# Kernel tuning notes

Hardware: AMD Instinct MI355X
Metric: run time of the kernel (lower is better)

The kernel has to match this reference:

```python
import jax, jax.numpy as jnp
import numpy as np

S0, S1 = 256, 256          # spins (up, down)
N = S0 + S1                # total electrons
SINGLE = 256               # single_dim == single_out (residual requires match)
PAIR = 128                 # pair_dim == pair_out
GAIN_TANH = 1.5927812698663017  # ActivationWithGain: 1/std(tanh(N(0,1)))
SQRT2 = 1.4142135623730951


def setup_inputs() -> dict:
    key = jax.random.key(0)
    ks = jax.random.split(key, 7)
    h_one = jax.random.normal(ks[0], (N, SINGLE), jnp.float32)
    h_two = jax.random.normal(ks[1], (N, N, PAIR), jnp.float32)
    din = SINGLE + 2 * PAIR  # one_in feature dim = 512
    # variance_scaling(2, fan_in) kernels; bias ~ Normal(0, sqrt(2))
    W1 = jax.random.normal(ks[2], (din, SINGLE), jnp.float32) * (2.0 / din) ** 0.5
    b1 = jax.random.normal(ks[3], (SINGLE,), jnp.float32) * SQRT2
    Wg = jax.random.normal(ks[4], (2 * SINGLE, SINGLE), jnp.float32) * (2.0 / (2 * SINGLE)) ** 0.5
    W2 = jax.random.normal(ks[5], (PAIR, PAIR), jnp.float32) * (2.0 / PAIR) ** 0.5
    b2 = jax.random.normal(ks[6], (PAIR,), jnp.float32) * SQRT2
    return dict(h_one=h_one, h_two=h_two, W1=W1, b1=b1, Wg=Wg, W2=W2, b2=b2)


def _act(x):
    # ActivationWithGain(tanh): rescale so output variance ~ input variance
    return jnp.tanh(x) * jnp.asarray(GAIN_TANH, x.dtype)


def reference(h_one, h_two, W1, b1, Wg, W2, b2):
    # construct_single_features: per-spin mean of h_two over sender axis
    g2_up = jnp.mean(h_two[:S0], axis=0)            # (N, PAIR)
    g2_dn = jnp.mean(h_two[S0:], axis=0)            # (N, PAIR)
    one_in = jnp.concatenate([h_one, g2_up, g2_dn], axis=1)   # (N, SINGLE+2*PAIR)
    # construct_global_features: per-spin mean of h_one, concat on features
    g1_up = jnp.mean(h_one[:S0], axis=0, keepdims=True)       # (1, SINGLE)
    g1_dn = jnp.mean(h_one[S0:], axis=0, keepdims=True)       # (1, SINGLE)
    global_in = jnp.concatenate([g1_up, g1_dn], axis=-1)      # (1, 2*SINGLE)

    h_one_new = one_in @ W1 + b1 + global_in @ Wg             # (N, SINGLE)
    h_one_new = _act(h_one_new / SQRT2)
    h_one_out = (h_one + h_one_new) / SQRT2                   # residual (shapes match)

    h_two_new = _act(h_two @ W2 + b2)                         # (N, N, PAIR)
    h_two_out = (h_two + h_two_new) / SQRT2                   # residual
    return h_one_out, h_two_out
```

## Files before the change

### kernel.cpp

```cpp
#include <hip/hip_runtime.h>
#include <stdint.h>

#define NN 512
#define PAIR 128
#define SINGLE 256

#define GAINv 1.5927812698663017f
#define RS2 0.70710678118654752f

typedef unsigned int uint;
typedef unsigned short ushort;
typedef short bf16x8 __attribute__((ext_vector_type(8)));
typedef float f32x4 __attribute__((ext_vector_type(4)));

__device__ __forceinline__ ushort f2b(float f){
  union{float f;uint i;}v; v.f=f;
  uint x=v.i;
  return (ushort)((x + 0x7FFFu + ((x>>16)&1u))>>16);
}
__device__ __forceinline__ float b2f_lo(uint u){ union{uint i;float f;}v; v.i=u<<16; return v.f; }
__device__ __forceinline__ float b2f_hi(uint u){ union{uint i;float f;}v; v.i=u&0xFFFF0000u; return v.f; }
__device__ __forceinline__ float tanh_fast(float x){
  float xc = fminf(fmaxf(x,-8.f),8.f);
  float e = __expf(2.f*xc);
  return (e-1.f)*__builtin_amdgcn_rcpf(e+1.f);
}

__global__ __launch_bounds__(256) void k1_prep(const float* __restrict__ h_one,
                                               const float* __restrict__ w2,
                                               float* __restrict__ g1part,
                                               ushort* __restrict__ wt,
                                               float* __restrict__ g2acc)
{
  const int b = blockIdx.x, t = threadIdx.x;
  if(b < 8){
    const int rb = b*64;
    float s = 0.f;
    for(int i=0;i<64;i++) s += h_one[(size_t)(rb+i)*SINGLE + t];
    g1part[b*SINGLE + t] = s;
  } else if(b < 16){
    const int bb = b-8;
    for(int e=t; e<16*128; e+=256){
      int kl = e>>7, n = e&127;
      int k = bb*16 + kl;
      wt[n*128 + k] = f2b(w2[(size_t)k*128 + n]);
    }
  } else {
    f32x4 z = (f32x4){0.f,0.f,0.f,0.f};
    f32x4* dst = (f32x4*)g2acc + (size_t)(b-16)*4096;
    for(int q=t; q<4096; q+=256) dst[q] = z;
  }
}

__global__ __launch_bounds__(256) void k2_gterm(const float* __restrict__ g1part,
                                                const float* __restrict__ wg,
                                                float* __restrict__ gtermpart)
{
  __shared__ float g1m[512];
  const int t = threadIdx.x;
  g1m[t]     = (g1part[t]      + g1part[256+t]  + g1part[512+t]  + g1part[768+t])  * (1.f/256.f);
  g1m[t+256] = (g1part[1024+t] + g1part[1280+t] + g1part[1536+t] + g1part[1792+t]) * (1.f/256.f);
  __syncthreads();
  const int fb = blockIdx.x*64;
  float s = 0.f;
  for(int f=fb; f<fb+64; f++)
    s += g1m[f]*wg[(size_t)f*SINGLE + t];
  gtermpart[blockIdx.x*SINGLE + t] = s;
}

__global__ __launch_bounds__(256, 4) void k3_htwo(
    const float* __restrict__ h_two,
    const float* __restrict__ b2,
    const ushort* __restrict__ wt,
    float* __restrict__ g2acc,
    float* __restrict__ out_h2)
{
  __shared__ __align__(16) ushort At[64*128];
  const int tid = threadIdx.x;
  const int w = tid>>6, lane = tid&63;
  const int lq = lane>>4, lr = lane&15;
  const int bi = blockIdx.x & 31, bj = blockIdx.x >> 5;
  const int i0 = bi*16, j0 = bj*4;
  const int spin = bi>>4;

  #pragma unroll
  for(int rep=0;rep<8;rep++){
    const int e = rep*1024 + tid*4;
    const int di = e>>9, c = e&511;
    const float4 v = *(const float4*)(h_two + ((size_t)(i0+di)*NN + j0)*PAIR + c);
    ushort4 pk; pk.x=f2b(v.x); pk.y=f2b(v.y); pk.z=f2b(v.z); pk.w=f2b(v.w);
    const int r = e>>7;
    *(ushort4*)(&At[e ^ ((r&7)<<3)]) = pk;
  }

  bf16x8 af[2][4];
  #pragma unroll
  for(int nt=0;nt<2;nt++){
    const int n = w*32 + nt*16 + lr;
    #pragma unroll
    for(int kk=0;kk<4;kk++)
      af[nt][kk] = *(const bf16x8*)(wt + n*128 + kk*32 + lq*8);
  }
  f32x4 bias[2];
  #pragma unroll
  for(int nt=0;nt<2;nt++){
    const float4 bv = *(const float4*)(b2 + w*32 + nt*16 + lq*4);
    bias[nt] = (f32x4){bv.x, bv.y, bv.z, bv.w};
  }
  __syncthreads();

  {
    const int dj = w, pp = lane;
    const uint* a32 = (const uint*)At;
    float s0=0.f, s1=0.f;
    #pragma unroll
    for(int di=0;di<16;di++){
      const int r = di*4+dj;
      uint u = a32[(r*64 + pp) ^ ((r&7)<<2)];
      s0 += b2f_lo(u); s1 += b2f_hi(u);
    }
    float* dst = g2acc + ((size_t)spin*NN + (j0+dj))*PAIR + pp*2;
    atomicAdd(dst, s0); atomicAdd(dst+1, s1);
  }

  f32x4 acc[4][2];
  #pragma unroll
  for(int mt=0;mt<4;mt++){
    acc[mt][0] = bias[0];
    acc[mt][1] = bias[1];
  }
  #pragma unroll
  for(int kk=0;kk<4;kk++){
    bf16x8 bfr[4];
    #pragma unroll
    for(int mt=0;mt<4;mt++){
      const int m = mt*16 + lr;
      const int e = m*128 + kk*32 + lq*8;
      bfr[mt] = *(const bf16x8*)(&At[e ^ ((lr&7)<<3)]);
    }
    #pragma unroll
    for(int mt=0;mt<4;mt++){
      acc[mt][0] = __builtin_amdgcn_mfma_f32_16x16x32_bf16(af[0][kk], bfr[mt], acc[mt][0], 0,0,0);
      acc[mt][1] = __builtin_amdgcn_mfma_f32_16x16x32_bf16(af[1][kk], bfr[mt], acc[mt][1], 0,0,0);
    }
  }

  #pragma unroll
  for(int mt=0;mt<4;mt++){
    const int m = mt*16 + lr;
    const size_t base = ((size_t)(i0 + (m>>2))*NN + (j0 + (m&3)))*PAIR;
    #pragma unroll
    for(int nt=0;nt<2;nt++){
      const int nb = w*32 + nt*16 + lq*4;
      const float4 rr = *(const float4*)(h_two + base + nb);
      f32x4 o;
      o[0] = (rr.x + GAINv*tanh_fast(acc[mt][nt][0]))*RS2;
      o[1] = (rr.y + GAINv*tanh_fast(acc[mt][nt][1]))*RS2;
      o[2] = (rr.z + GAINv*tanh_fast(acc[mt][nt][2]))*RS2;
      o[3] = (rr.w + GAINv*tanh_fast(acc[mt][nt][3]))*RS2;
      *(f32x4*)(out_h2 + base + nb) = o;
    }
  }
}

__global__ __launch_bounds__(256) void k4_hone(
    const float* __restrict__ h_one,
    const float* __restrict__ w1,
    const float* __restrict__ b1,
    const float* __restrict__ g2acc,
    const float* __restrict__ gtermpart,
    float* __restrict__ out_h1)
{
  __shared__ float onein[2][512];
  const int n  = threadIdx.x;
  const int r0 = blockIdx.x*2;
  #pragma unroll
  for(int rr=0; rr<2; rr++){
    onein[rr][n] = h_one[(size_t)(r0+rr)*SINGLE + n];
    int sp = n>>7, p = n&127;
    onein[rr][256+n] = g2acc[((size_t)sp*NN + (r0+rr))*PAIR + p] * (1.f/256.f);
  }
  float gt = 0.f;
  #pragma unroll
  for(int bb=0;bb<8;bb++) gt += gtermpart[bb*256+n];
  __syncthreads();
  float a0=0.f, a1=0.f;
  for(int f=0; f<512; f++){
    float wv = w1[(size_t)f*SINGLE + n];
    a0 += onein[0][f]*wv;
    a1 += onein[1][f]*wv;
  }
  const float bn = b1[n];
  float x0 = (a0 + bn + gt)*RS2;
  float x1 = (a1 + bn + gt)*RS2;
  out_h1[(size_t)r0*SINGLE + n]     = (onein[0][n] + GAINv*tanh_fast(x0))*RS2;
  out_h1[(size_t)(r0+1)*SINGLE + n] = (onein[1][n] + GAINv*tanh_fast(x1))*RS2;
}

extern "C" void kernel_launch(void* const* d_in, const int* in_sizes, int n_in,
                              void* d_out, int out_size, void* d_ws, size_t ws_size,
                              hipStream_t stream)
{
  const float* h_one = (const float*)d_in[0];
  const float* h_two = (const float*)d_in[1];
  const float* W1    = (const float*)d_in[2];
  const float* b1    = (const float*)d_in[3];
  const float* Wg    = (const float*)d_in[4];
  const float* W2    = (const float*)d_in[5];
  const float* b2    = (const float*)d_in[6];

  float* wsf       = (float*)d_ws;
  float* g2acc     = wsf;
  ushort* wt       = (ushort*)(wsf + 131072);
  float* g1part    = wsf + 139264;
  float* gtermpart = wsf + 141312;

  float* out_h1 = (float*)d_out;
  float* out_h2 = out_h1 + 131072;

  k1_prep <<<24,   256, 0, stream>>>(h_one, W2, g1part, wt, g2acc);
  k2_gterm<<<8,    256, 0, stream>>>(g1part, Wg, gtermpart);
  k3_htwo <<<4096, 256, 0, stream>>>(h_two, b2, wt, g2acc, out_h2);
  k4_hone <<<256,  256, 0, stream>>>(h_one, W1, b1, g2acc, gtermpart, out_h1);
}
```

Before: 314.7 us.

## Make h_two kernel persistent over four j-tiles with double-buffered LDS prefetch

The main pair kernel now runs 1024 blocks, each looping over four j-tiles. The next tile's global loads go into registers while the current tile's MFMA and epilogue run, and the data is written to a second LDS buffer before one barrier per tile. The aim is to hide global-load latency and spread the W2 fragment and bias loads over more work. The cost is more LDS (double buffer) and register pressure, which may cut occupancy. The single-feature kernel also switches to one row per block with twice as many blocks, trading W1 reuse for more parallelism.

Result: slower. 344.7 us (+9.6%).

```diff
diff --git a/kernel.cpp b/kernel.cpp
--- a/kernel.cpp
+++ b/kernel.cpp
@@ -75,24 +75,23 @@
     float* __restrict__ g2acc,
     float* __restrict__ out_h2)
 {
-  __shared__ __align__(16) ushort At[64*128];
+  __shared__ __align__(16) ushort At[2][64*128];
   const int tid = threadIdx.x;
   const int w = tid>>6, lane = tid&63;
   const int lq = lane>>4, lr = lane&15;
-  const int bi = blockIdx.x & 31, bj = blockIdx.x >> 5;
-  const int i0 = bi*16, j0 = bj*4;
+  const int bi = blockIdx.x & 31;
+  const int bjg = blockIdx.x >> 5;
+  const int i0 = bi*16;
+  const int j0base = bjg*16;
   const int spin = bi>>4;
 
+  float4 L[8];
   #pragma unroll
   for(int rep=0;rep<8;rep++){
     const int e = rep*1024 + tid*4;
     const int di = e>>9, c = e&511;
-    const float4 v = *(const float4*)(h_two + ((size_t)(i0+di)*NN + j0)*PAIR + c);
-    ushort4 pk; pk.x=f2b(v.x); pk.y=f2b(v.y); pk.z=f2b(v.z); pk.w=f2b(v.w);
-    const int r = e>>7;
-    *(ushort4*)(&At[e ^ ((r&7)<<3)]) = pk;
-  }
-
+    L[rep] = *(const float4*)(h_two + ((size_t)(i0+di)*NN + j0base)*PAIR + c);
+  }
   bf16x8 af[2][4];
   #pragma unroll
   for(int nt=0;nt<2;nt++){
@@ -107,58 +106,82 @@
     const float4 bv = *(const float4*)(b2 + w*32 + nt*16 + lq*4);
     bias[nt] = (f32x4){bv.x, bv.y, bv.z, bv.w};
   }
+  #pragma unroll
+  for(int rep=0;rep<8;rep++){
+    const int e = rep*1024 + tid*4;
+    const int r = e>>7;
+    ushort4 pk; pk.x=f2b(L[rep].x); pk.y=f2b(L[rep].y); pk.z=f2b(L[rep].z); pk.w=f2b(L[rep].w);
+    *(ushort4*)(&At[0][e ^ ((r&7)<<3)]) = pk;
+  }
   __syncthreads();
 
-  {
-    const int dj = w, pp = lane;
-    const uint* a32 = (const uint*)At;
-    float s0=0.f, s1=0.f;
-    #pragma unroll
-    for(int di=0;di<16;di++){
-      const int r = di*4+dj;
-      uint u = a32[(r*64 + pp) ^ ((r&7)<<2)];
-      s0 += b2f_lo(u); s1 += b2f_hi(u);
-    }
-    float* dst = g2acc + ((size_t)spin*NN + (j0+dj))*PAIR + pp*2;
-    atomicAdd(dst, s0); atomicAdd(dst+1, s1);
-  }
-
-  f32x4 acc[4][2];
-  #pragma unroll
-  for(int mt=0;mt<4;mt++){
-    acc[mt][0] = bias[0];
-    acc[mt][1] = bias[1];
-  }
-  #pragma unroll
-  for(int kk=0;kk<4;kk++){
-    bf16x8 bfr[4];
-    #pragma unroll
-    for(int mt=0;mt<4;mt++){
-      const int m = mt*16 + lr;
-      const int e = m*128 + kk*32 + lq*8;
-      bfr[mt] = *(const bf16x8*)(&At[e ^ ((lr&7)<<3)]);
-    }
-    #pragma unroll
-    for(int mt=0;mt<4;mt++){
-      acc[mt][0] = __builtin_amdgcn_mfma_f32_16x16x32_bf16(af[0][kk], bfr[mt], acc[mt][0], 0,0,0);
-      acc[mt][1] = __builtin_amdgcn_mfma_f32_16x16x32_bf16(af[1][kk], bfr[mt], acc[mt][1], 0,0,0);
-    }
-  }
-
-  #pragma unroll
-  for(int mt=0;mt<4;mt++){
-    const int m = mt*16 + lr;
-    const size_t base = ((size_t)(i0 + (m>>2))*NN + (j0 + (m&3)))*PAIR;
+  #pragma unroll
+  for(int t=0;t<4;t++){
+    const int j0 = j0base + t*4;
+    const ushort* cur = &At[t&1][0];
+
+    if(t<3){
+      #pragma unroll
+      for(int rep=0;rep<8;rep++){
+        const int e = rep*1024 + tid*4;
+        const int di = e>>9, c = e&511;
+        L[rep] = *(const float4*)(h_two + ((size_t)(i0+di)*NN + (j0+4))*PAIR + c);
+      }
+    }
+
+    {
+      const uint* a32 = (const uint*)cur;
+      float s0=0.f, s1=0.f;
+      #pragma unroll
+      for(int di=0;di<16;di++){
+        const int r = di*4+w;
+        uint u = a32[(r*64 + lane) ^ ((r&7)<<2)];
+        s0 += b2f_lo(u); s1 += b2f_hi(u);
+      }
+      float* dst = g2acc + ((size_t)spin*NN + (j0+w))*PAIR + lane*2;
+      atomicAdd(dst, s0); atomicAdd(dst+1, s1);
+    }
+
     #pragma unroll
     for(int nt=0;nt<2;nt++){
-      const int nb = w*32 + nt*16 + lq*4;
-      const float4 rr = *(const float4*)(h_two + base + nb);
-      f32x4 o;
-      o[0] = (rr.x + GAINv*tanh_fast(acc[mt][nt][0]))*RS2;
-      o[1] = (rr.y + GAINv*tanh_fast(acc[mt][nt][1]))*RS2;
-      o[2] = (rr.z + GAINv*tanh_fast(acc[mt][nt][2]))*RS2;
-      o[3] = (rr.w + GAINv*tanh_fast(acc[mt][nt][3]))*RS2;
-      *(f32x4*)(out_h2 + base + nb) = o;
+      f32x4 acc[4];
+      #pragma unroll
+      for(int mt=0;mt<4;mt++) acc[mt] = bias[nt];
+      #pragma unroll
+      for(int kk=0;kk<4;kk++){
+        #pragma unroll
+        for(int mt=0;mt<4;mt++){
+          const int m = mt*16 + lr;
+          const int e = m*128 + kk*32 + lq*8;
+          const bf16x8 bfr = *(const bf16x8*)(&cur[e ^ ((lr&7)<<3)]);
+          acc[mt] = __builtin_amdgcn_mfma_f32_16x16x32_bf16(af[nt][kk], bfr, acc[mt], 0,0,0);
+        }
+      }
+      #pragma unroll
+      for(int mt=0;mt<4;mt++){
+        const int m = mt*16 + lr;
+        const size_t base = ((size_t)(i0 + (m>>2))*NN + (j0 + (m&3)))*PAIR;
+        const int nb = w*32 + nt*16 + lq*4;
+        const float4 rr = *(const float4*)(h_two + base + nb);
+        f32x4 o;
+        o[0] = (rr.x + GAINv*tanh_fast(acc[mt][0]))*RS2;
+        o[1] = (rr.y + GAINv*tanh_fast(acc[mt][1]))*RS2;
+        o[2] = (rr.z + GAINv*tanh_fast(acc[mt][2]))*RS2;
+        o[3] = (rr.w + GAINv*tanh_fast(acc[mt][3]))*RS2;
+        *(f32x4*)(out_h2 + base + nb) = o;
+      }
+    }
+
+    if(t<3){
+      ushort* nxt = &At[(t+1)&1][0];
+      #pragma unroll
+      for(int rep=0;rep<8;rep++){
+        const int e = rep*1024 + tid*4;
+        const int r = e>>7;
+        ushort4 pk; pk.x=f2b(L[rep].x); pk.y=f2b(L[rep].y); pk.z=f2b(L[rep].z); pk.w=f2b(L[rep].w);
+        *(ushort4*)(&nxt[e ^ ((r&7)<<3)]) = pk;
+      }
+      __syncthreads();
     }
   }
 }
@@ -171,30 +194,23 @@
     const float* __restrict__ gtermpart,
     float* __restrict__ out_h1)
 {
-  __shared__ float onein[2][512];
-  const int n  = threadIdx.x;
-  const int r0 = blockIdx.x*2;
-  #pragma unroll
-  for(int rr=0; rr<2; rr++){
-    onein[rr][n] = h_one[(size_t)(r0+rr)*SINGLE + n];
+  __shared__ float onein[512];
+  const int n   = threadIdx.x;
+  const int row = blockIdx.x;
+  onein[n] = h_one[(size_t)row*SINGLE + n];
+  {
     int sp = n>>7, p = n&127;
-    onein[rr][256+n] = g2acc[((size_t)sp*NN + (r0+rr))*PAIR + p] * (1.f/256.f);
+    onein[256+n] = g2acc[((size_t)sp*NN + row)*PAIR + p] * (1.f/256.f);
   }
   float gt = 0.f;
   #pragma unroll
   for(int bb=0;bb<8;bb++) gt += gtermpart[bb*256+n];
   __syncthreads();
-  float a0=0.f, a1=0.f;
-  for(int f=0; f<512; f++){
-    float wv = w1[(size_t)f*SINGLE + n];
-    a0 += onein[0][f]*wv;
-    a1 += onein[1][f]*wv;
-  }
-  const float bn = b1[n];
-  float x0 = (a0 + bn + gt)*RS2;
-  float x1 = (a1 + bn + gt)*RS2;
-  out_h1[(size_t)r0*SINGLE + n]     = (onein[0][n] + GAINv*tanh_fast(x0))*RS2;
-  out_h1[(size_t)(r0+1)*SINGLE + n] = (onein[1][n] + GAINv*tanh_fast(x1))*RS2;
+  float a = 0.f;
+  for(int f=0; f<512; f++)
+    a += onein[f] * w1[(size_t)f*SINGLE + n];
+  float x = (a + b1[n] + gt) * RS2;
+  out_h1[(size_t)row*SINGLE + n] = (onein[n] + GAINv*tanh_fast(x)) * RS2;
 }
 
 extern "C" void kernel_launch(void* const* d_in, const int* in_sizes, int n_in,
@@ -220,6 +236,6 @@
 
   k1_prep <<<24,   256, 0, stream>>>(h_one, W2, g1part, wt, g2acc);
   k2_gterm<<<8,    256, 0, stream>>>(g1part, Wg, gtermpart);
-  k3_htwo <<<4096, 256, 0, stream>>>(h_two, b2, wt, g2acc, out_h2);
-  k4_hone <<<256,  256, 0, stream>>>(h_one, W1, b1, g2acc, gtermpart, out_h1);
-}
+  k3_htwo <<<1024, 256, 0, stream>>>(h_two, b2, wt, g2acc, out_h2);
+  k4_hone <<<512,  256, 0, stream>>>(h_one, W1, b1, g2acc, gtermpart, out_h1);
+}
```
